# Kernel optimization log

Hardware: AMD Instinct MI355X
Metric: run time of the kernel (lower is better)

The kernel has to match this reference:

```python
import jax, jax.numpy as jnp
import numpy as np

H, KD, VD = 8, 64, 64
W = 1.25  # custom weight scale


def layer_norm(x, g, b, eps=1e-5):
    m = x.mean(-1, keepdims=True)
    v = ((x - m) ** 2).mean(-1, keepdims=True)
    return (x - m) * jax.lax.rsqrt(v + eps) * g + b


def cross_attention(x1, x2, wq, wk, wv, wo, bo, wm):
    # Conv1d kernel_size=1 == matmul; channel axis splits as (heads, dim)
    b, s1, _ = x1.shape
    s2 = x2.shape[1]
    q = (x1 @ wq.T).reshape(b, s1, H, KD).transpose(0, 2, 1, 3)  # bhqk
    k = (x2 @ wk.T).reshape(b, s2, H, KD).transpose(0, 2, 1, 3)
    v = (x2 @ wv.T).reshape(b, s2, H, VD).transpose(0, 2, 1, 3)
    attn = jnp.einsum('bhqd,bhsd->bhqs', q, k) * (1.0 / (KD ** 0.5))
    attn = jax.nn.softmax(attn * wm, axis=-1)  # elementwise weight BEFORE softmax
    o = jnp.einsum('bhqs,bhsv->bhqv', attn, v)
    o = o.transpose(0, 2, 1, 3).reshape(b, s1, H * VD)
    return o @ wo.T + bo


def make_wm1(nvars, sl2, patch_num):
    sl = sl2 // 2
    wm = jnp.ones((nvars, sl2), jnp.float32)
    wm = wm.at[:2 * patch_num, :sl].multiply(W)
    wm = wm.at[2 * patch_num:, sl:].multiply(W)
    return wm[None, None]  # broadcast over batch, heads


def make_wm2(nvars, sv, patch_num, patch_num_v):
    wm = jnp.ones((nvars, sv), jnp.float32)
    wm = wm.at[:patch_num, :patch_num_v].multiply(W)
    wm = wm.at[patch_num:2 * patch_num, patch_num_v:2 * patch_num_v].multiply(W)
    wm = wm.at[2 * patch_num:, 2 * patch_num_v:].multiply(W)
    return wm[None, None]


def forward(cords_features, spatial_features, speed_features,
            wq1, wk1, wv1, wo1, bo1, wq2, wk2, wv2, wo2, bo2,
            ln1_g, ln1_b, ln2_g, ln2_b, ln3_g, ln3_b,
            ffn_w1, ffn_b1, ffn_w2, ffn_b2):
    b, nvars, d = cords_features.shape
    patch_num = nvars // 3
    patch_num_v = speed_features.shape[1] // 3
    wm1 = make_wm1(nvars, spatial_features.shape[1], patch_num)
    wm2 = make_wm2(nvars, 3 * patch_num_v, patch_num, patch_num_v)
    x = cross_attention(cords_features, spatial_features, wq1, wk1, wv1, wo1, bo1, wm1)
    x = layer_norm(x + cords_features, ln1_g, ln1_b)
    r2 = x
    x = cross_attention(x, speed_features, wq2, wk2, wv2, wo2, bo2, wm2)
    x = layer_norm(x + r2, ln2_g, ln2_b)
    r3 = x
    h = jax.nn.gelu(x @ ffn_w1.T + ffn_b1, approximate=False)
    x = h @ ffn_w2.T + ffn_b2
    return layer_norm(x + r3, ln3_g, ln3_b)


def setup_inputs():
    key = jax.random.key(0)
    ks = jax.random.split(key, 16)
    D, DF = 512, 2048
    s = 0.02
    inp = {
        'cords_features': jax.random.normal(ks[0], (8, 768, D), jnp.float32),
        'spatial_features': jax.random.normal(ks[1], (8, 1024, D), jnp.float32),
        'speed_features': jax.random.normal(ks[2], (8, 768, D), jnp.float32),
        'wq1': jax.random.normal(ks[3], (H * KD, D)) * s,
        'wk1': jax.random.normal(ks[4], (H * KD, D)) * s,
        'wv1': jax.random.normal(ks[5], (H * VD, D)) * s,
        'wo1': jax.random.normal(ks[6], (D, H * VD)) * s,
        'bo1': jnp.zeros((D,), jnp.float32),
        'wq2': jax.random.normal(ks[7], (H * KD, D)) * s,
        'wk2': jax.random.normal(ks[8], (H * KD, D)) * s,
        'wv2': jax.random.normal(ks[9], (H * VD, D)) * s,
        'wo2': jax.random.normal(ks[10], (D, H * VD)) * s,
        'bo2': jnp.zeros((D,), jnp.float32),
        'ln1_g': jnp.ones((D,), jnp.float32), 'ln1_b': jnp.zeros((D,), jnp.float32),
        'ln2_g': jnp.ones((D,), jnp.float32), 'ln2_b': jnp.zeros((D,), jnp.float32),
        'ln3_g': jnp.ones((D,), jnp.float32), 'ln3_b': jnp.zeros((D,), jnp.float32),
        'ffn_w1': jax.random.normal(ks[11], (DF, D)) * s,
        'ffn_b1': jnp.zeros((DF,), jnp.float32),
        'ffn_w2': jax.random.normal(ks[12], (D, DF)) * s,
        'ffn_b2': jnp.zeros((D,), jnp.float32),
    }
    return inp


def reference(cords_features, spatial_features, speed_features,
              wq1, wk1, wv1, wo1, bo1, wq2, wk2, wv2, wo2, bo2,
              ln1_g, ln1_b, ln2_g, ln2_b, ln3_g, ln3_b,
              ffn_w1, ffn_b1, ffn_w2, ffn_b2):
    return forward(cords_features, spatial_features, speed_features,
                   wq1, wk1, wv1, wo1, bo1, wq2, wk2, wv2, wo2, bo2,
                   ln1_g, ln1_b, ln2_g, ln2_b, ln3_g, ln3_b,
                   ffn_w1, ffn_b1, ffn_w2, ffn_b2)
```

## Files before the change

### kernel.cpp

```cpp
#include <hip/hip_runtime.h>
#include <hip/hip_bf16.h>


#define LN_EPS 1e-5f
#define WSCALE 1.25f

typedef __attribute__((ext_vector_type(8))) short short8;
typedef __attribute__((ext_vector_type(4))) float floatx4;
typedef unsigned short us;

__device__ __forceinline__ float bf2f(us u) {
    union { unsigned int i; float f; } v; v.i = ((unsigned int)u) << 16; return v.f;
}
__device__ __forceinline__ us f2bf(float f) {
    union { float f; unsigned int i; } v; v.f = f;
    return (us)((v.i + 0x7FFFu + ((v.i >> 16) & 1u)) >> 16);
}
__device__ __forceinline__ float gelu_f(float v) {
    float x  = v * 0.70710678118654752f;
    float ax = fabsf(x);
    float t  = 1.0f / (1.0f + 0.3275911f * ax);
    float p  = t * (0.254829592f + t * (-0.284496736f + t * (1.421413741f +
               t * (-1.453152027f + t * 1.061405429f))));
    float er = 1.0f - p * __expf(-ax * ax);
    er = copysignf(er, x);
    return 0.5f * v * (1.0f + er);
}

struct CastArgs {
    const float* src[13];
    us* dst[13];
    int blk_ofs[14];
};
__global__ __launch_bounds__(256) void cast_all(CastArgs a)
{
    int b = blockIdx.x;
    int e = 0;
    while (b >= a.blk_ofs[e + 1]) ++e;
    int i = ((b - a.blk_ofs[e]) * 256 + threadIdx.x) * 8;
    const float* s = a.src[e];
    us* d = a.dst[e];
    float4 x = *(const float4*)(s + i);
    float4 y = *(const float4*)(s + i + 4);
    *(ushort4*)(d + i)     = make_ushort4(f2bf(x.x), f2bf(x.y), f2bf(x.z), f2bf(x.w));
    *(ushort4*)(d + i + 4) = make_ushort4(f2bf(y.x), f2bf(y.y), f2bf(y.z), f2bf(y.w));
}

__global__ __launch_bounds__(256) void gemm64(
    const us* __restrict__ A, const us* __restrict__ Bw,
    const float* __restrict__ bias, us* __restrict__ Cb,
    int M, int N, int K, int flags)
{
    __shared__ us As[2][64 * 64];
    __shared__ us Bs[2][64 * 64];

    int t = threadIdx.x;
    int wave = t >> 6, lane = t & 63;
    int m0 = blockIdx.y * 64, n0 = blockIdx.x * 64;
    int wr = (wave >> 1) * 32, wc = (wave & 1) * 32;

    int r_in = lane >> 3;
    int pq   = lane & 7;
    const us* gA[2]; const us* gB[2];
    int lofs[2];
#pragma unroll
    for (int c = 0; c < 2; ++c) {
        int r = 16 * wave + 8 * c + r_in;
        int q = pq ^ (r & 7);
        gA[c] = A  + (size_t)(m0 + r) * K + 8 * q;
        gB[c] = Bw + (size_t)(n0 + r) * K + 8 * q;
        lofs[c] = (16 * wave + 8 * c) * 64;
    }

    int fcol = lane & 15, fj = lane >> 4;
    int aoff[2][2], boff[2][2];
#pragma unroll
    for (int mt = 0; mt < 2; ++mt)
#pragma unroll
        for (int kc = 0; kc < 2; ++kc) {
            int fr = wr + 16 * mt + fcol;
            aoff[mt][kc] = fr * 64 + ((kc * 4 + fj) ^ (fr & 7)) * 8;
            int br = wc + 16 * mt + fcol;
            boff[mt][kc] = br * 64 + ((kc * 4 + fj) ^ (br & 7)) * 8;
        }

    floatx4 acc[2][2] = {};

    auto stage = [&](int buf, int k0) {
#pragma unroll
        for (int c = 0; c < 2; ++c) {
            __builtin_amdgcn_global_load_lds(
                (const __attribute__((address_space(1))) void*)(gA[c] + k0),
                (__attribute__((address_space(3))) void*)(As[buf] + lofs[c]), 16, 0, 0);
            __builtin_amdgcn_global_load_lds(
                (const __attribute__((address_space(1))) void*)(gB[c] + k0),
                (__attribute__((address_space(3))) void*)(Bs[buf] + lofs[c]), 16, 0, 0);
        }
    };

    int ktrips = K >> 6;
    stage(0, 0);
    for (int tt = 0; tt < ktrips; ++tt) {
        int buf = tt & 1;
        if (tt + 1 < ktrips) {
            stage(buf ^ 1, (tt + 1) << 6);
            asm volatile("s_waitcnt vmcnt(4)" ::: "memory");
        } else {
            asm volatile("s_waitcnt vmcnt(0)" ::: "memory");
        }
        __builtin_amdgcn_s_barrier();
        asm volatile("" ::: "memory");

        const us* as_ = As[buf];
        const us* bs_ = Bs[buf];
        short8 af[2][2], bfr[2][2];
#pragma unroll
        for (int mt = 0; mt < 2; ++mt)
#pragma unroll
            for (int kc = 0; kc < 2; ++kc) {
                af[mt][kc]  = *(const short8*)(as_ + aoff[mt][kc]);
                bfr[mt][kc] = *(const short8*)(bs_ + boff[mt][kc]);
            }
#pragma unroll
        for (int kc = 0; kc < 2; ++kc)
#pragma unroll
            for (int mt = 0; mt < 2; ++mt)
#pragma unroll
                for (int nt = 0; nt < 2; ++nt)
                    acc[mt][nt] = __builtin_amdgcn_mfma_f32_16x16x32_bf16(
                        af[mt][kc], bfr[nt][kc], acc[mt][nt], 0, 0, 0);

        asm volatile("" ::: "memory");
        __builtin_amdgcn_s_barrier();
    }

    int rq = lane >> 4;
#pragma unroll
    for (int mt = 0; mt < 2; ++mt)
#pragma unroll
        for (int nt = 0; nt < 2; ++nt) {
            int col = n0 + wc + 16 * nt + fcol;
            float bv = (flags & 1) ? bias[col] : 0.f;
#pragma unroll
            for (int r = 0; r < 4; ++r) {
                int row = m0 + wr + 16 * mt + rq * 4 + r;
                Cb[(size_t)row * N + col] = f2bf(acc[mt][nt][r] + bv);
            }
        }
}

template<int BM, int BN>
__global__ __launch_bounds__(512, 2) void gemm_ring(
    const us* __restrict__ A, const us* __restrict__ Bw,
    const float* __restrict__ bias, us* __restrict__ Cb,
    int M, int N, int K, int flags, int vS, us* __restrict__ Vtg)
{
    static_assert(BM == 256 && BN == 128, "gemm_ring fixed at 256x128");
    constexpr int SLOT = (BM + BN) * 64;
    __shared__ us L[3 * SLOT];

    int t = threadIdx.x;
    int wave = t >> 6, lane = t & 63;
    int m0 = blockIdx.y * BM, n0 = blockIdx.x * BN;
    int wr = (wave >> 1) * 64, wc = (wave & 1) * 64;

    int r_in = lane >> 3, pq = lane & 7;
    const us* gA[4]; int lA[4];
#pragma unroll
    for (int c = 0; c < 4; ++c) {
        int r = 64 * c + 8 * wave + r_in;
        int q = pq ^ (r & 7);
        gA[c] = A + (size_t)(m0 + r) * K + 8 * q;
        lA[c] = (64 * c + 8 * wave) * 64;
    }
    const us* gB[2]; int lB[2];
#pragma unroll
    for (int c = 0; c < 2; ++c) {
        int r = 64 * c + 8 * wave + r_in;
        int q = pq ^ (r & 7);
        gB[c] = Bw + (size_t)(n0 + r) * K + 8 * q;
        lB[c] = BM * 64 + (64 * c + 8 * wave) * 64;
    }

    int fcol = lane & 15, fj = lane >> 4;
    int aoff[4][2], boff[4][2];
#pragma unroll
    for (int mt = 0; mt < 4; ++mt)
#pragma unroll
        for (int kc = 0; kc < 2; ++kc) {
            int fr = wr + 16 * mt + fcol;
            aoff[mt][kc] = fr * 64 + ((kc * 4 + fj) ^ (fr & 7)) * 8;
        }
#pragma unroll
    for (int nt = 0; nt < 4; ++nt)
#pragma unroll
        for (int kc = 0; kc < 2; ++kc) {
            int br = wc + 16 * nt + fcol;
            boff[nt][kc] = BM * 64 + br * 64 + ((kc * 4 + fj) ^ (br & 7)) * 8;
        }

    floatx4 acc[4][4] = {};

    auto stage_p0 = [&](int slot, int kt) {
        us* base = L + slot * SLOT;
#pragma unroll
        for (int c = 0; c < 3; ++c)
            __builtin_amdgcn_global_load_lds(
                (const __attribute__((address_space(1))) void*)(gA[c] + (size_t)kt * 64),
                (__attribute__((address_space(3))) void*)(base + lA[c]), 16, 0, 0);
    };
    auto stage_p1 = [&](int slot, int kt) {
        us* base = L + slot * SLOT;
        __builtin_amdgcn_global_load_lds(
            (const __attribute__((address_space(1))) void*)(gA[3] + (size_t)kt * 64),
            (__attribute__((address_space(3))) void*)(base + lA[3]), 16, 0, 0);
#pragma unroll
        for (int c = 0; c < 2; ++c)
            __builtin_amdgcn_global_load_lds(
                (const __attribute__((address_space(1))) void*)(gB[c] + (size_t)kt * 64),
                (__attribute__((address_space(3))) void*)(base + lB[c]), 16, 0, 0);
    };

    int ktrips = K >> 6;
    stage_p0(0, 0); stage_p1(0, 0);
    if (ktrips > 1) {
        stage_p0(1, 1); stage_p1(1, 1);
        asm volatile("s_waitcnt vmcnt(6)" ::: "memory");
    } else {
        asm volatile("s_waitcnt vmcnt(0)" ::: "memory");
    }
    __builtin_amdgcn_s_barrier();
    asm volatile("" ::: "memory");

    int cs = 0;
    for (int tt = 0; tt < ktrips; ++tt) {
        int ns = cs + 2; if (ns >= 3) ns -= 3;
        bool pre = (tt + 2) < ktrips;
        const us* base = L + cs * SLOT;

        if (pre) stage_p0(ns, tt + 2);
        {
            short8 af[4], bfv[4];
#pragma unroll
            for (int mt = 0; mt < 4; ++mt) af[mt] = *(const short8*)(base + aoff[mt][0]);
#pragma unroll
            for (int nt = 0; nt < 4; ++nt) bfv[nt] = *(const short8*)(base + boff[nt][0]);
            __builtin_amdgcn_s_setprio(1);
#pragma unroll
            for (int mt = 0; mt < 4; ++mt)
#pragma unroll
                for (int nt = 0; nt < 4; ++nt)
                    acc[mt][nt] = __builtin_amdgcn_mfma_f32_16x16x32_bf16(
                        af[mt], bfv[nt], acc[mt][nt], 0, 0, 0);
            __builtin_amdgcn_s_setprio(0);
        }

        if (pre) stage_p1(ns, tt + 2);
        {
            short8 af[4], bfv[4];
#pragma unroll
            for (int mt = 0; mt < 4; ++mt) af[mt] = *(const short8*)(base + aoff[mt][1]);
#pragma unroll
            for (int nt = 0; nt < 4; ++nt) bfv[nt] = *(const short8*)(base + boff[nt][1]);
            __builtin_amdgcn_s_setprio(1);
#pragma unroll
            for (int mt = 0; mt < 4; ++mt)
#pragma unroll
                for (int nt = 0; nt < 4; ++nt)
                    acc[mt][nt] = __builtin_amdgcn_mfma_f32_16x16x32_bf16(
                        af[mt], bfv[nt], acc[mt][nt], 0, 0, 0);
            __builtin_amdgcn_s_setprio(0);
        }

        if (tt + 1 < ktrips) {
            if (pre) asm volatile("s_waitcnt vmcnt(6)" ::: "memory");
            else     asm volatile("s_waitcnt vmcnt(0)" ::: "memory");
            __builtin_amdgcn_s_barrier();
            asm volatile("" ::: "memory");
        }
        cs = cs + 1; if (cs >= 3) cs = 0;
    }

    int rq = lane >> 4;
    if (flags & 8) {
        int b = m0 / vS;
        int s_base = m0 - b * vS;
        if (n0 < 512) {
#pragma unroll
            for (int mt = 0; mt < 4; ++mt)
#pragma unroll
                for (int nt = 0; nt < 4; ++nt) {
                    int col = n0 + wc + 16 * nt + fcol;
#pragma unroll
                    for (int r = 0; r < 4; ++r) {
                        int rloc = wr + 16 * mt + rq * 4 + r;
                        Cb[(size_t)(m0 + rloc) * 512 + col] = f2bf(acc[mt][nt][r]);
                    }
                }
        } else {
#pragma unroll
            for (int mt = 0; mt < 4; ++mt)
#pragma unroll
                for (int nt = 0; nt < 4; ++nt) {
                    int cv = n0 + wc + 16 * nt + fcol - 512;
                    int hv = cv >> 6, dv = cv & 63;
                    int sb = s_base + wr + 16 * mt + rq * 4;
                    ushort4 pk = make_ushort4(
                        f2bf(acc[mt][nt][0]), f2bf(acc[mt][nt][1]),
                        f2bf(acc[mt][nt][2]), f2bf(acc[mt][nt][3]));
                    *(ushort4*)(Vtg + ((size_t)(b * 8 + hv) * 64 + dv) * vS + sb) = pk;
                }
        }
        return;
    }

#pragma unroll
    for (int mt = 0; mt < 4; ++mt)
#pragma unroll
        for (int nt = 0; nt < 4; ++nt) {
            int col = n0 + wc + 16 * nt + fcol;
            float bv = (flags & 1) ? bias[col] : 0.f;
#pragma unroll
            for (int r = 0; r < 4; ++r) {
                int row = m0 + wr + 16 * mt + rq * 4 + r;
                float v = acc[mt][nt][r] + bv;
                if (flags & 2) v = gelu_f(v);
                Cb[(size_t)row * N + col] = f2bf(v);
            }
        }
}

__global__ __launch_bounds__(256, 3) void attn_kernel(
    const us* __restrict__ Q, const us* __restrict__ Kf,
    const us* __restrict__ Vg, us* __restrict__ O,
    int S1, int S2, int shift)
{
    __shared__ us Qs[64 * 64];
    __shared__ us Ks[2][64 * 64];
    __shared__ us Vs[2][64 * 64];
    __shared__ us Ps[64 * 72];

    int t = threadIdx.x;
    int wave = t >> 6, lane = t & 63;
    int quad = lane >> 4, l15 = lane & 15;
    int q0 = blockIdx.x * 64, hh = blockIdx.y, bb = blockIdx.z;
    int qb = wave * 16;

    int r_in = lane >> 3, pq = lane & 7;
    const us *gK[2], *gV[2];
    int lofs[2];
#pragma unroll
    for (int c2 = 0; c2 < 2; ++c2) {
        int r = qb + 8 * c2 + r_in;
        int lq = pq ^ (r & 7);
        const us* gQ = Q + ((size_t)bb * S1 + q0 + r) * 512 + hh * 64 + 8 * lq;
        gK[c2] = Kf + ((size_t)bb * S2 + r) * 512 + hh * 64 + 8 * lq;
        gV[c2] = Vg + ((size_t)(bb * 8 + hh) * 64 + r) * S2 + 8 * lq;
        lofs[c2] = (qb + 8 * c2) * 64;
        __builtin_amdgcn_global_load_lds(
            (const __attribute__((address_space(1))) void*)gQ,
            (__attribute__((address_space(3))) void*)(Qs + lofs[c2]), 16, 0, 0);
    }

    int aoffQ[2], poffP[2], boff[4][2];
#pragma unroll
    for (int kc = 0; kc < 2; ++kc) {
        int ph = ((kc * 4 + quad) ^ (l15 & 7)) * 8;
        aoffQ[kc] = (qb + l15) * 64 + ph;
        poffP[kc] = (qb + l15) * 72 + ph;
#pragma unroll
        for (int nt = 0; nt < 4; ++nt)
            boff[nt][kc] = (16 * nt + l15) * 64 + ph;
    }
    int pwoff[4][4];
#pragma unroll
    for (int r = 0; r < 4; ++r) {
        int row = qb + quad * 4 + r;
#pragma unroll
        for (int nt = 0; nt < 4; ++nt) {
            int s = 16 * nt + l15;
            pwoff[nt][r] = row * 72 + (((s >> 3) ^ (row & 7)) * 8) + (s & 7);
        }
    }

    floatx4 acc_o[4] = {};
    float l_part[4] = {0.f, 0.f, 0.f, 0.f};
    int qsh[4];
#pragma unroll
    for (int r = 0; r < 4; ++r) qsh[r] = (q0 + qb + quad * 4 + r) >> shift;

    auto stageKV = [&](int buf, int cc) {
#pragma unroll
        for (int c2 = 0; c2 < 2; ++c2) {
            __builtin_amdgcn_global_load_lds(
                (const __attribute__((address_space(1))) void*)(gK[c2] + (size_t)cc * 512),
                (__attribute__((address_space(3))) void*)(Ks[buf] + lofs[c2]), 16, 0, 0);
            __builtin_amdgcn_global_load_lds(
                (const __attribute__((address_space(1))) void*)(gV[c2] + cc),
                (__attribute__((address_space(3))) void*)(Vs[buf] + lofs[c2]), 16, 0, 0);
        }
    };

    stageKV(0, 0);
    asm volatile("s_waitcnt vmcnt(4)" ::: "memory");
    __builtin_amdgcn_s_barrier();
    asm volatile("" ::: "memory");
    short8 aq0 = *(const short8*)(Qs + aoffQ[0]);
    short8 aq1 = *(const short8*)(Qs + aoffQ[1]);

    int ntile = S2 >> 6;
    for (int ti = 0; ti < ntile; ++ti) {
        int buf = ti & 1;
        if (ti + 1 < ntile) {
            stageKV(buf ^ 1, (ti + 1) << 6);
            asm volatile("s_waitcnt vmcnt(4)" ::: "memory");
        } else {
            asm volatile("s_waitcnt vmcnt(0)" ::: "memory");
        }
        __builtin_amdgcn_s_barrier();
        asm volatile("" ::: "memory");

        const us* ks_ = Ks[buf];
        const us* vs_ = Vs[buf];
        int cbase = ti << 6;

        floatx4 s_acc[4] = {};
#pragma unroll
        for (int nt = 0; nt < 4; ++nt) {
            short8 bk0 = *(const short8*)(ks_ + boff[nt][0]);
            short8 bk1 = *(const short8*)(ks_ + boff[nt][1]);
            s_acc[nt] = __builtin_amdgcn_mfma_f32_16x16x32_bf16(aq0, bk0, s_acc[nt], 0, 0, 0);
            s_acc[nt] = __builtin_amdgcn_mfma_f32_16x16x32_bf16(aq1, bk1, s_acc[nt], 0, 0, 0);
        }

#pragma unroll
        for (int nt = 0; nt < 4; ++nt) {
            int srs = (cbase + 16 * nt + l15) >> shift;
#pragma unroll
            for (int r = 0; r < 4; ++r) {
                float fct = (qsh[r] == srs) ? (0.125f * WSCALE) : 0.125f;
                float p = __expf(s_acc[nt][r] * fct);
                s_acc[nt][r] = p;
                l_part[r] += p;
            }
        }

#pragma unroll
        for (int nt = 0; nt < 4; ++nt)
#pragma unroll
            for (int r = 0; r < 4; ++r)
                Ps[pwoff[nt][r]] = f2bf(s_acc[nt][r]);
        __builtin_amdgcn_wave_barrier();

        short8 ap0 = *(const short8*)(Ps + poffP[0]);
        short8 ap1 = *(const short8*)(Ps + poffP[1]);
#pragma unroll
        for (int nt = 0; nt < 4; ++nt) {
            short8 bv0 = *(const short8*)(vs_ + boff[nt][0]);
            short8 bv1 = *(const short8*)(vs_ + boff[nt][1]);
            acc_o[nt] = __builtin_amdgcn_mfma_f32_16x16x32_bf16(ap0, bv0, acc_o[nt], 0, 0, 0);
            acc_o[nt] = __builtin_amdgcn_mfma_f32_16x16x32_bf16(ap1, bv1, acc_o[nt], 0, 0, 0);
        }

        asm volatile("" ::: "memory");
        __builtin_amdgcn_s_barrier();
    }

#pragma unroll
    for (int r = 0; r < 4; ++r) {
#pragma unroll
        for (int off = 8; off; off >>= 1)
            l_part[r] += __shfl_xor(l_part[r], off, 16);
    }
#pragma unroll
    for (int r = 0; r < 4; ++r) {
        float inv = 1.0f / l_part[r];
        size_t base = ((size_t)bb * S1 + q0 + qb + quad * 4 + r) * 512 + hh * 64;
#pragma unroll
        for (int nt = 0; nt < 4; ++nt)
            O[base + 16 * nt + l15] = f2bf(acc_o[nt][r] * inv);
    }
}

__global__ __launch_bounds__(256) void ln_kernel(
    const us* __restrict__ X, const float* __restrict__ R,
    const float* __restrict__ g, const float* __restrict__ bta,
    float* __restrict__ out, us* __restrict__ outb)
{
    int row = blockIdx.x;
    int t   = threadIdx.x;
    const us*    xr = X + (size_t)row * 512;
    const float* rr = R + (size_t)row * 512;
    float v0 = bf2f(xr[t]) + rr[t];
    float v1 = bf2f(xr[t + 256]) + rr[t + 256];
    float s  = v0 + v1;
    float sq = v0 * v0 + v1 * v1;
#pragma unroll
    for (int off = 32; off; off >>= 1) {
        s  += __shfl_xor(s, off, 64);
        sq += __shfl_xor(sq, off, 64);
    }
    __shared__ float ps[4], psq[4];
    int w = t >> 6;
    if ((t & 63) == 0) { ps[w] = s; psq[w] = sq; }
    __syncthreads();
    float S  = ps[0] + ps[1] + ps[2] + ps[3];
    float SQ = psq[0] + psq[1] + psq[2] + psq[3];
    float mean = S * (1.0f / 512.0f);
    float var  = SQ * (1.0f / 512.0f) - mean * mean;
    float inv  = rsqrtf(var + LN_EPS);
    float y0 = (v0 - mean) * inv * g[t] + bta[t];
    float y1 = (v1 - mean) * inv * g[t + 256] + bta[t + 256];
    out[(size_t)row * 512 + t]       = y0;
    out[(size_t)row * 512 + t + 256] = y1;
    if (outb) {
        outb[(size_t)row * 512 + t]       = f2bf(y0);
        outb[(size_t)row * 512 + t + 256] = f2bf(y1);
    }
}

extern "C" void kernel_launch(void* const* d_in, const int* in_sizes, int n_in,
                              void* d_out, int out_size, void* d_ws, size_t ws_size,
                              hipStream_t stream)
{
    const float* cords   = (const float*)d_in[0];
    const float* spatial = (const float*)d_in[1];
    const float* speed   = (const float*)d_in[2];
    const float* wq1 = (const float*)d_in[3];
    const float* wk1 = (const float*)d_in[4];
    const float* wv1 = (const float*)d_in[5];
    const float* wo1 = (const float*)d_in[6];
    const float* bo1 = (const float*)d_in[7];
    const float* wq2 = (const float*)d_in[8];
    const float* wk2 = (const float*)d_in[9];
    const float* wv2 = (const float*)d_in[10];
    const float* wo2 = (const float*)d_in[11];
    const float* bo2 = (const float*)d_in[12];
    const float* ln1g = (const float*)d_in[13];
    const float* ln1b = (const float*)d_in[14];
    const float* ln2g = (const float*)d_in[15];
    const float* ln2b = (const float*)d_in[16];
    const float* ln3g = (const float*)d_in[17];
    const float* ln3b = (const float*)d_in[18];
    const float* fw1 = (const float*)d_in[19];
    const float* fb1 = (const float*)d_in[20];
    const float* fw2 = (const float*)d_in[21];
    const float* fb2 = (const float*)d_in[22];

    const int B = 8, S1 = 768, S2 = 1024, Sv = 768, D = 512, DF = 2048;
    const int M1 = B * S1;
    const int M2 = B * S2;

    char* w = (char*)d_ws;
    us* q_bf = (us*)w;              w += (size_t)M1 * D * 2;
    us* k_bf = (us*)w;              w += (size_t)M2 * D * 2;
    us* vt   = (us*)w;              w += (size_t)M2 * D * 2;
    us* o_bf = (us*)w;              w += (size_t)M1 * D * 2;
    us* p_bf = (us*)w;              w += (size_t)M1 * D * 2;
    float* x1 = (float*)w;          w += (size_t)M1 * D * 4;
    us* cords_bf   = (us*)w;        w += (size_t)M1 * D * 2;
    us* spatial_bf = (us*)w;        w += (size_t)M2 * D * 2;
    us* speed_bf   = (us*)w;        w += (size_t)M1 * D * 2;
    us* wq1b = (us*)w;              w += (size_t)D * D * 2;
    us* wk1b = (us*)w;              w += (size_t)D * D * 2;
    us* wv1b = (us*)w;              w += (size_t)D * D * 2;
    us* wo1b = (us*)w;              w += (size_t)D * D * 2;
    us* wq2b = (us*)w;              w += (size_t)D * D * 2;
    us* wk2b = (us*)w;              w += (size_t)D * D * 2;
    us* wv2b = (us*)w;              w += (size_t)D * D * 2;
    us* wo2b = (us*)w;              w += (size_t)D * D * 2;
    us* fw1b = (us*)w;              w += (size_t)DF * D * 2;
    us* fw2b = (us*)w;              w += (size_t)DF * D * 2;

    us* h_bf  = q_bf;
    us* y_bf  = p_bf;
    us* x1_bf = spatial_bf;
    us* x2_bf = cords_bf;
    float* x2 = (float*)d_out;

    dim3 blk(256);
    dim3 blk512(512);

    {
        CastArgs ca;
        const float* srcs[13] = {cords, spatial, speed, wq1, wk1, wv1, wo1,
                                 wq2, wk2, wv2, wo2, fw1, fw2};
        us* dsts[13] = {cords_bf, spatial_bf, speed_bf, wq1b, wk1b, wv1b, wo1b,
                        wq2b, wk2b, wv2b, wo2b, fw1b, fw2b};
        int ns[13] = {M1 * D, M2 * D, M1 * D, D * D, D * D, D * D, D * D,
                      D * D, D * D, D * D, D * D, DF * D, DF * D};
        int ofs = 0;
        for (int i = 0; i < 13; ++i) {
            ca.src[i] = srcs[i]; ca.dst[i] = dsts[i];
            ca.blk_ofs[i] = ofs; ofs += ns[i] / 2048;
        }
        ca.blk_ofs[13] = ofs;
        cast_all<<<dim3(ofs), blk, 0, stream>>>(ca);
    }

    auto g64   = [](int M, int N) { return dim3(N / 64,  M / 64); };
    auto gring = [](int M, int N) { return dim3(N / 128, M / 256); };

    gemm64<<<g64(M1, D), blk, 0, stream>>>(cords_bf, wq1b, nullptr, q_bf, M1, D, D, 0);
    gemm_ring<256, 128><<<gring(M2, 1024), blk512, 0, stream>>>(spatial_bf, wk1b, nullptr, k_bf,
                                                                M2, 1024, D, 8, S2, vt);
    attn_kernel<<<dim3(S1 / 64, 8, B), blk, 0, stream>>>(q_bf, k_bf, vt, o_bf, S1, S2, 9);
    gemm64<<<g64(M1, D), blk, 0, stream>>>(o_bf, wo1b, bo1, p_bf, M1, D, D, 1);
    ln_kernel<<<M1, blk, 0, stream>>>(p_bf, cords, ln1g, ln1b, x1, x1_bf);

    gemm64<<<g64(M1, D), blk, 0, stream>>>(x1_bf, wq2b, nullptr, q_bf, M1, D, D, 0);
    gemm_ring<256, 128><<<gring(M1, 1024), blk512, 0, stream>>>(speed_bf, wk2b, nullptr, k_bf,
                                                                M1, 1024, D, 8, Sv, vt);
    attn_kernel<<<dim3(S1 / 64, 8, B), blk, 0, stream>>>(q_bf, k_bf, vt, o_bf, S1, Sv, 8);
    gemm64<<<g64(M1, D), blk, 0, stream>>>(o_bf, wo2b, bo2, p_bf, M1, D, D, 1);
    ln_kernel<<<M1, blk, 0, stream>>>(p_bf, x1, ln2g, ln2b, x2, x2_bf);

    gemm_ring<256, 128><<<gring(M1, DF), blk512, 0, stream>>>(x2_bf, fw1b, fb1, h_bf,
                                                              M1, DF, D, 1 | 2 | 4, 0, nullptr);
    gemm64<<<g64(M1, D), blk, 0, stream>>>(h_bf, fw2b, fb2, y_bf, M1, D, DF, 1);
    ln_kernel<<<M1, blk, 0, stream>>>(y_bf, x2, ln3g, ln3b, (float*)d_out, nullptr);

    (void)in_sizes; (void)n_in; (void)out_size; (void)ws_size;
}
```

Baseline: 353.7 us.

## Replace gemm64 with 128x64 triple-buffered ring GEMM and XCD-aware block swizzle

```diff
diff --git a/kernel.cpp b/kernel.cpp
--- a/kernel.cpp
+++ b/kernel.cpp
@@ -25,6 +25,14 @@
     float er = 1.0f - p * __expf(-ax * ax);
     er = copysignf(er, x);
     return 0.5f * v * (1.0f + er);
+}
+
+__device__ __forceinline__ int xcd_swizzle_lid()
+{
+    int nwg = gridDim.x * gridDim.y;
+    int lid = blockIdx.y * gridDim.x + blockIdx.x;
+    int cpx = nwg >> 3;
+    return (lid & 7) * cpx + (lid >> 3);
 }
 
 struct CastArgs {
@@ -46,105 +54,154 @@
     *(ushort4*)(d + i + 4) = make_ushort4(f2bf(y.x), f2bf(y.y), f2bf(y.z), f2bf(y.w));
 }
 
-__global__ __launch_bounds__(256) void gemm64(
+__global__ __launch_bounds__(256) void gemm_r64(
     const us* __restrict__ A, const us* __restrict__ Bw,
     const float* __restrict__ bias, us* __restrict__ Cb,
     int M, int N, int K, int flags)
 {
-    __shared__ us As[2][64 * 64];
-    __shared__ us Bs[2][64 * 64];
+    constexpr int BM = 128, BN = 64;
+    constexpr int SLOT = (BM + BN) * 64;
+    __shared__ us L[3 * SLOT];
 
     int t = threadIdx.x;
     int wave = t >> 6, lane = t & 63;
-    int m0 = blockIdx.y * 64, n0 = blockIdx.x * 64;
-    int wr = (wave >> 1) * 32, wc = (wave & 1) * 32;
-
-    int r_in = lane >> 3;
-    int pq   = lane & 7;
-    const us* gA[2]; const us* gB[2];
-    int lofs[2];
+
+    int swz = xcd_swizzle_lid();
+    int gx = gridDim.x;
+    int m0 = (swz / gx) * BM, n0 = (swz % gx) * BN;
+
+    int wr = wave * 32;
+
+    int r_in = lane >> 3, pq = lane & 7;
+    const us* gA[4]; int lA[4];
+#pragma unroll
+    for (int c = 0; c < 4; ++c) {
+        int r = 32 * c + 8 * wave + r_in;
+        int q = pq ^ (r & 7);
+        gA[c] = A + (size_t)(m0 + r) * K + 8 * q;
+        lA[c] = (32 * c + 8 * wave) * 64;
+    }
+    const us* gB[2]; int lB[2];
 #pragma unroll
     for (int c = 0; c < 2; ++c) {
-        int r = 16 * wave + 8 * c + r_in;
+        int r = 32 * c + 8 * wave + r_in;
         int q = pq ^ (r & 7);
-        gA[c] = A  + (size_t)(m0 + r) * K + 8 * q;
         gB[c] = Bw + (size_t)(n0 + r) * K + 8 * q;
-        lofs[c] = (16 * wave + 8 * c) * 64;
+        lB[c] = BM * 64 + (32 * c + 8 * wave) * 64;
     }
 
     int fcol = lane & 15, fj = lane >> 4;
-    int aoff[2][2], boff[2][2];
+    int aoff[2][2], boff[4][2];
 #pragma unroll
     for (int mt = 0; mt < 2; ++mt)
 #pragma unroll
         for (int kc = 0; kc < 2; ++kc) {
             int fr = wr + 16 * mt + fcol;
             aoff[mt][kc] = fr * 64 + ((kc * 4 + fj) ^ (fr & 7)) * 8;
-            int br = wc + 16 * mt + fcol;
-            boff[mt][kc] = br * 64 + ((kc * 4 + fj) ^ (br & 7)) * 8;
-        }
-
-    floatx4 acc[2][2] = {};
-
-    auto stage = [&](int buf, int k0) {
-#pragma unroll
-        for (int c = 0; c < 2; ++c) {
+        }
+#pragma unroll
+    for (int nt = 0; nt < 4; ++nt)
+#pragma unroll
+        for (int kc = 0; kc < 2; ++kc) {
+            int br = 16 * nt + fcol;
+            boff[nt][kc] = BM * 64 + br * 64 + ((kc * 4 + fj) ^ (br & 7)) * 8;
+        }
+
+    floatx4 acc[2][4] = {};
+
+    auto stage_p0 = [&](int slot, int kt) {
+        us* base = L + slot * SLOT;
+#pragma unroll
+        for (int c = 0; c < 3; ++c)
             __builtin_amdgcn_global_load_lds(
-                (const __attribute__((address_space(1))) void*)(gA[c] + k0),
-                (__attribute__((address_space(3))) void*)(As[buf] + lofs[c]), 16, 0, 0);
+                (const __attribute__((address_space(1))) void*)(gA[c] + (size_t)kt * 64),
+                (__attribute__((address_space(3))) void*)(base + lA[c]), 16, 0, 0);
+    };
+    auto stage_p1 = [&](int slot, int kt) {
+        us* base = L + slot * SLOT;
+        __builtin_amdgcn_global_load_lds(
+            (const __attribute__((address_space(1))) void*)(gA[3] + (size_t)kt * 64),
+            (__attribute__((address_space(3))) void*)(base + lA[3]), 16, 0, 0);
+#pragma unroll
+        for (int c = 0; c < 2; ++c)
             __builtin_amdgcn_global_load_lds(
-                (const __attribute__((address_space(1))) void*)(gB[c] + k0),
-                (__attribute__((address_space(3))) void*)(Bs[buf] + lofs[c]), 16, 0, 0);
-        }
+                (const __attribute__((address_space(1))) void*)(gB[c] + (size_t)kt * 64),
+                (__attribute__((address_space(3))) void*)(base + lB[c]), 16, 0, 0);
     };
 
     int ktrips = K >> 6;
-    stage(0, 0);
+    stage_p0(0, 0); stage_p1(0, 0);
+    if (ktrips > 1) {
+        stage_p0(1, 1); stage_p1(1, 1);
+        asm volatile("s_waitcnt vmcnt(6)" ::: "memory");
+    } else {
+        asm volatile("s_waitcnt vmcnt(0)" ::: "memory");
+    }
+    __builtin_amdgcn_s_barrier();
+    asm volatile("" ::: "memory");
+
+    int cs = 0;
     for (int tt = 0; tt < ktrips; ++tt) {
-        int buf = tt & 1;
+        int ns = cs + 2; if (ns >= 3) ns -= 3;
+        bool pre = (tt + 2) < ktrips;
+        const us* base = L + cs * SLOT;
+
+        if (pre) stage_p0(ns, tt + 2);
+        {
+            short8 af[2], bfv[4];
+#pragma unroll
+            for (int mt = 0; mt < 2; ++mt) af[mt] = *(const short8*)(base + aoff[mt][0]);
+#pragma unroll
+            for (int nt = 0; nt < 4; ++nt) bfv[nt] = *(const short8*)(base + boff[nt][0]);
+            __builtin_amdgcn_s_setprio(1);
+#pragma unroll
+            for (int mt = 0; mt < 2; ++mt)
+#pragma unroll
+                for (int nt = 0; nt < 4; ++nt)
+                    acc[mt][nt] = __builtin_amdgcn_mfma_f32_16x16x32_bf16(
+                        af[mt], bfv[nt], acc[mt][nt], 0, 0, 0);
+            __builtin_amdgcn_s_setprio(0);
+        }
+
+        if (pre) stage_p1(ns, tt + 2);
+        {
+            short8 af[2], bfv[4];
+#pragma unroll
+            for (int mt = 0; mt < 2; ++mt) af[mt] = *(const short8*)(base + aoff[mt][1]);
+#pragma unroll
+            for (int nt = 0; nt < 4; ++nt) bfv[nt] = *(const short8*)(base + boff[nt][1]);
+            __builtin_amdgcn_s_setprio(1);
+#pragma unroll
+            for (int mt = 0; mt < 2; ++mt)
+#pragma unroll
+                for (int nt = 0; nt < 4; ++nt)
+                    acc[mt][nt] = __builtin_amdgcn_mfma_f32_16x16x32_bf16(
+                        af[mt], bfv[nt], acc[mt][nt], 0, 0, 0);
+            __builtin_amdgcn_s_setprio(0);
+        }
+
         if (tt + 1 < ktrips) {
-            stage(buf ^ 1, (tt + 1) << 6);
-            asm volatile("s_waitcnt vmcnt(4)" ::: "memory");
-        } else {
-            asm volatile("s_waitcnt vmcnt(0)" ::: "memory");
-        }
-        __builtin_amdgcn_s_barrier();
-        asm volatile("" ::: "memory");
-
-        const us* as_ = As[buf];
-        const us* bs_ = Bs[buf];
-        short8 af[2][2], bfr[2][2];
-#pragma unroll
-        for (int mt = 0; mt < 2; ++mt)
-#pragma unroll
-            for (int kc = 0; kc < 2; ++kc) {
-                af[mt][kc]  = *(const short8*)(as_ + aoff[mt][kc]);
-                bfr[mt][kc] = *(const short8*)(bs_ + boff[mt][kc]);
-            }
-#pragma unroll
-        for (int kc = 0; kc < 2; ++kc)
-#pragma unroll
-            for (int mt = 0; mt < 2; ++mt)
-#pragma unroll
-                for (int nt = 0; nt < 2; ++nt)
-                    acc[mt][nt] = __builtin_amdgcn_mfma_f32_16x16x32_bf16(
-                        af[mt][kc], bfr[nt][kc], acc[mt][nt], 0, 0, 0);
-
-        asm volatile("" ::: "memory");
-        __builtin_amdgcn_s_barrier();
+            if (pre) asm volatile("s_waitcnt vmcnt(6)" ::: "memory");
+            else     asm volatile("s_waitcnt vmcnt(0)" ::: "memory");
+            __builtin_amdgcn_s_barrier();
+            asm volatile("" ::: "memory");
+        }
+        cs = cs + 1; if (cs >= 3) cs = 0;
     }
 
     int rq = lane >> 4;
 #pragma unroll
     for (int mt = 0; mt < 2; ++mt)
 #pragma unroll
-        for (int nt = 0; nt < 2; ++nt) {
-            int col = n0 + wc + 16 * nt + fcol;
+        for (int nt = 0; nt < 4; ++nt) {
+            int col = n0 + 16 * nt + fcol;
             float bv = (flags & 1) ? bias[col] : 0.f;
 #pragma unroll
             for (int r = 0; r < 4; ++r) {
                 int row = m0 + wr + 16 * mt + rq * 4 + r;
-                Cb[(size_t)row * N + col] = f2bf(acc[mt][nt][r] + bv);
+                float v = acc[mt][nt][r] + bv;
+                if (flags & 2) v = gelu_f(v);
+                Cb[(size_t)row * N + col] = f2bf(v);
             }
         }
 }
@@ -161,7 +218,11 @@
 
     int t = threadIdx.x;
     int wave = t >> 6, lane = t & 63;
-    int m0 = blockIdx.y * BM, n0 = blockIdx.x * BN;
+
+    int swz = xcd_swizzle_lid();
+    int gx = gridDim.x;
+    int m0 = (swz / gx) * BM, n0 = (swz % gx) * BN;
+
     int wr = (wave >> 1) * 64, wc = (wave & 1) * 64;
 
     int r_in = lane >> 3, pq = lane & 7;
@@ -598,26 +659,26 @@
         cast_all<<<dim3(ofs), blk, 0, stream>>>(ca);
     }
 
-    auto g64   = [](int M, int N) { return dim3(N / 64,  M / 64); };
+    auto gr64  = [](int M, int N) { return dim3(N / 64,  M / 128); };
     auto gring = [](int M, int N) { return dim3(N / 128, M / 256); };
 
-    gemm64<<<g64(M1, D), blk, 0, stream>>>(cords_bf, wq1b, nullptr, q_bf, M1, D, D, 0);
+    gemm_r64<<<gr64(M1, D), blk, 0, stream>>>(cords_bf, wq1b, nullptr, q_bf, M1, D, D, 0);
     gemm_ring<256, 128><<<gring(M2, 1024), blk512, 0, stream>>>(spatial_bf, wk1b, nullptr, k_bf,
                                                                 M2, 1024, D, 8, S2, vt);
     attn_kernel<<<dim3(S1 / 64, 8, B), blk, 0, stream>>>(q_bf, k_bf, vt, o_bf, S1, S2, 9);
-    gemm64<<<g64(M1, D), blk, 0, stream>>>(o_bf, wo1b, bo1, p_bf, M1, D, D, 1);
+    gemm_r64<<<gr64(M1, D), blk, 0, stream>>>(o_bf, wo1b, bo1, p_bf, M1, D, D, 1);
     ln_kernel<<<M1, blk, 0, stream>>>(p_bf, cords, ln1g, ln1b, x1, x1_bf);
 
-    gemm64<<<g64(M1, D), blk, 0, stream>>>(x1_bf, wq2b, nullptr, q_bf, M1, D, D, 0);
+    gemm_r64<<<gr64(M1, D), blk, 0, stream>>>(x1_bf, wq2b, nullptr, q_bf, M1, D, D, 0);
     gemm_ring<256, 128><<<gring(M1, 1024), blk512, 0, stream>>>(speed_bf, wk2b, nullptr, k_bf,
                                                                 M1, 1024, D, 8, Sv, vt);
     attn_kernel<<<dim3(S1 / 64, 8, B), blk, 0, stream>>>(q_bf, k_bf, vt, o_bf, S1, Sv, 8);
-    gemm64<<<g64(M1, D), blk, 0, stream>>>(o_bf, wo2b, bo2, p_bf, M1, D, D, 1);
+    gemm_r64<<<gr64(M1, D), blk, 0, stream>>>(o_bf, wo2b, bo2, p_bf, M1, D, D, 1);
     ln_kernel<<<M1, blk, 0, stream>>>(p_bf, x1, ln2g, ln2b, x2, x2_bf);
 
     gemm_ring<256, 128><<<gring(M1, DF), blk512, 0, stream>>>(x2_bf, fw1b, fb1, h_bf,
                                                               M1, DF, D, 1 | 2 | 4, 0, nullptr);
-    gemm64<<<g64(M1, D), blk, 0, stream>>>(h_bf, fw2b, fb2, y_bf, M1, D, DF, 1);
+    gemm_r64<<<gr64(M1, D), blk, 0, stream>>>(h_bf, fw2b, fb2, y_bf, M1, D, DF, 1);
     ln_kernel<<<M1, blk, 0, stream>>>(y_bf, x2, ln3g, ln3b, (float*)d_out, nullptr);
 
     (void)in_sizes; (void)n_in; (void)out_size; (void)ws_size;
```

After: 333.7 us. 1.06x faster.
